# Kernel tuning notes

Measured on AMD Instinct MI355X. Metric: run time of the kernel, lower is better.

Reference implementation:

```python
import jax, jax.numpy as jnp
import numpy as np

L, B, H, R = 128, 4, 768, 24
LN_EPS = 1e-5


def setup_inputs() -> dict:
    key = jax.random.key(0)
    ks = jax.random.split(key, 10)
    s = 1.0 / np.sqrt(H)
    return {
        "h_re": jax.random.normal(ks[0], (L, B, H), jnp.float32),
        "h_share": jax.random.normal(ks[1], (L, B, H), jnp.float32),
        "mask": jnp.ones((L, B), jnp.float32),
        # r: Linear(2H -> H)
        "r_w": jax.random.normal(ks[2], (H, 2 * H), jnp.float32) * s,
        "r_b": jnp.zeros((H,), jnp.float32),
        # hid2hid: Linear(3H -> H)
        "hid_w": jax.random.normal(ks[3], (H, 3 * H), jnp.float32) * s,
        "hid_b": jnp.zeros((H,), jnp.float32),
        # LayerNorm(H)
        "ln_g": jnp.ones((H,), jnp.float32),
        "ln_b": jnp.zeros((H,), jnp.float32),
        # hid2rel: Linear(H -> R)
        "rel_w": jax.random.normal(ks[4], (R, H), jnp.float32) * s,
        "rel_b": jnp.zeros((R,), jnp.float32),
    }


def reference(h_re, h_share, mask, r_w, r_b, hid_w, hid_b, ln_g, ln_b, rel_w, rel_b):
    # h_global = max_over_length( tanh( Linear([h_share; h_re]) ) )  -> [B, H]
    # Decompose concat-linear into two additive projections (same math).
    w_sh, w_re = r_w[:, :H], r_w[:, H:]
    g = jnp.tanh(jnp.einsum('lbh,kh->lbk', h_share, w_sh)
                 + jnp.einsum('lbh,kh->lbk', h_re, w_re) + r_b)
    g = jnp.max(g, axis=0)  # [B, H]

    # hid2hid(cat(r1, r2, g)) = h_re@W1^T (bcast over j) + h_re@W2^T (bcast over i) + g@W3^T + b
    w1, w2, w3 = hid_w[:, :H], hid_w[:, H:2 * H], hid_w[:, 2 * H:]
    p1 = jnp.einsum('lbh,kh->lbk', h_re, w1)        # [L, B, H] -> varies with i
    p2 = jnp.einsum('lbh,kh->lbk', h_re, w2)        # [L, B, H] -> varies with j
    pg = jnp.einsum('bh,kh->bk', g, w3) + hid_b     # [B, H]
    z = p1[:, None, :, :] + p2[None, :, :, :] + pg  # [L, L, B, H]

    # LayerNorm over last dim
    mu = jnp.mean(z, axis=-1, keepdims=True)
    var = jnp.mean(jnp.square(z - mu), axis=-1, keepdims=True)
    z = (z - mu) * jax.lax.rsqrt(var + LN_EPS) * ln_g + ln_b

    # ELU (dropout = identity in eval), then sigmoid(hid2rel)
    z = jax.nn.elu(z)
    re = jax.nn.sigmoid(jnp.einsum('ijbh,rh->ijbr', z, rel_w) + rel_b)  # [L, L, B, R]

    # pairwise mask: mask[i,b] * mask[j,b]
    m = mask[:, None, :] * mask[None, :, :]        # [L, L, B]
    return re * m[..., None]
```

## Files before the change

kernel.cpp:

```cpp
#include <hip/hip_runtime.h>
#include <hip/hip_bf16.h>
#include <math.h>

#define L 128
#define B 4
#define H 768
#define LN_EPS 1e-5f
#define XROWS 272
#define DSTRIDE 73984

typedef __attribute__((ext_vector_type(8))) short short8;
typedef __attribute__((ext_vector_type(4))) float f32x4;
typedef __attribute__((ext_vector_type(16))) float f32x16;

static __device__ __forceinline__ unsigned f2bfu(float f) {
    unsigned u = __float_as_uint(f);
    return (u + 0x7FFFu + ((u >> 16) & 1u)) >> 16;
}
static __device__ __forceinline__ uint2 pk4(float4 v) {
    uint2 o;
    o.x = f2bfu(v.x) | (f2bfu(v.y) << 16);
    o.y = f2bfu(v.z) | (f2bfu(v.w) << 16);
    return o;
}
static __device__ __forceinline__ unsigned short f2b(float f) {
    union { __hip_bfloat16 h; unsigned short u; } cv;
    cv.h = __float2bfloat16(f);
    return cv.u;
}
static __device__ __forceinline__ float4 unpk4(uint2 p) {
    return make_float4(__uint_as_float(p.x << 16),
                       __uint_as_float(p.x & 0xffff0000u),
                       __uint_as_float(p.y << 16),
                       __uint_as_float(p.y & 0xffff0000u));
}
static __device__ __forceinline__ unsigned fkey(float x) {
    unsigned u = __float_as_uint(x);
    return (u >> 31) ? ~u : (u | 0x80000000u);
}

__global__ __launch_bounds__(256) void kConv(const float* __restrict__ h_re,
                                             const float* __restrict__ h_share,
                                             const float* __restrict__ r_w,
                                             const float* __restrict__ hid_w,
                                             const float* __restrict__ rel_w,
                                             unsigned short* __restrict__ apack,
                                             unsigned short* __restrict__ wpackA,
                                             unsigned short* __restrict__ wpackB,
                                             unsigned short* __restrict__ rwb2,
                                             unsigned short* __restrict__ xb16,
                                             unsigned int* __restrict__ gmax) {
    int t = blockIdx.x * 256 + threadIdx.x;
    if (t >= 402816) return;
    if (t < 98304) {
        int m = t / 192, oct = t % 192, k = oct * 8;
        const float* src = (k < 768) ? (h_share + (size_t)m * 768 + k)
                                     : (h_re + (size_t)m * 768 + k - 768);
        float4 x = *(const float4*)src, y = *(const float4*)(src + 4);
        int mt = m >> 4, lr = m & 15, ks = k >> 5, lq = (k >> 3) & 3;
        uint2* dst = (uint2*)(apack + (((size_t)mt * 48 + ks) * 64 + lq * 16 + lr) * 8);
        dst[0] = pk4(x); dst[1] = pk4(y);
    } else if (t < 245760) {
        int t2 = t - 98304;
        int n = t2 / 192, oct = t2 % 192, k = oct * 8;
        const float* src = r_w + (size_t)n * 1536 + k;
        float4 x = *(const float4*)src, y = *(const float4*)(src + 4);
        int nt = n >> 4, lr = n & 15, ks = k >> 5, lq = (k >> 3) & 3;
        uint2* dst = (uint2*)(wpackA + (((size_t)nt * 48 + ks) * 64 + lq * 16 + lr) * 8);
        dst[0] = pk4(x); dst[1] = pk4(y);
    } else if (t < 393216) {
        int t3 = t - 245760;
        int n = t3 / 96, oct = t3 % 96, k = oct * 8;
        int half = (n >= 768) ? 1 : 0;
        const float* src = hid_w + (size_t)(n - half * 768) * 2304 + half * 768 + k;
        float4 x = *(const float4*)src, y = *(const float4*)(src + 4);
        int nt = n >> 4, lr = n & 15, ks = k >> 5, lq = (k >> 3) & 3;
        uint2* dst = (uint2*)(wpackB + (((size_t)nt * 24 + ks) * 64 + lq * 16 + lr) * 8);
        dst[0] = pk4(x); dst[1] = pk4(y);
    } else if (t < 396288) {
        int t4 = t - 393216;
        int s = t4 >> 6, l = t4 & 63;
        int row = l & 31;
        uint2 o0 = make_uint2(0u, 0u), o1 = o0;
        if (row < 24) {
            const float* src = rel_w + (size_t)row * 768 + s * 16 + (l >> 5) * 8;
            o0 = pk4(*(const float4*)src);
            o1 = pk4(*(const float4*)(src + 4));
        }
        uint2* dst = (uint2*)(rwb2 + (size_t)t4 * 8);
        dst[0] = o0; dst[1] = o1;
    } else if (t < 402048) {
        int t5 = t - 396288;
        int b = t5 / 1440, rem = t5 % 1440, row = 257 + rem / 96, oct = rem % 96;
        unsigned val = (row == 257) ? 0x3F803F80u : 0u;
        uint2* dst = (uint2*)(xb16 + ((size_t)b * XROWS + row) * 768 + oct * 8);
        dst[0] = make_uint2(val, val); dst[1] = make_uint2(val, val);
    } else {
        int t6 = t - 402048;
        ((uint4*)gmax)[t6] = make_uint4(0u, 0u, 0u, 0u);
    }
}

template<int KS>
static __device__ __forceinline__ void gemm_tile(const unsigned short* __restrict__ ap,
                                                 const unsigned short* __restrict__ wr,
                                                 f32x4 acc[2][2]) {
#pragma unroll 8
    for (int s = 0; s < KS; s++) {
        short8 a0 = *(const short8*)(ap + (size_t)s * 512);
        short8 a1 = *(const short8*)(ap + (size_t)(48 + s) * 512);
        short8 w0 = *(const short8*)(wr + (size_t)s * 512);
        short8 w1 = *(const short8*)(wr + (size_t)(KS + s) * 512);
        acc[0][0] = __builtin_amdgcn_mfma_f32_16x16x32_bf16(a0, w0, acc[0][0], 0, 0, 0);
        acc[0][1] = __builtin_amdgcn_mfma_f32_16x16x32_bf16(a0, w1, acc[0][1], 0, 0, 0);
        acc[1][0] = __builtin_amdgcn_mfma_f32_16x16x32_bf16(a1, w0, acc[1][0], 0, 0, 0);
        acc[1][1] = __builtin_amdgcn_mfma_f32_16x16x32_bf16(a1, w1, acc[1][1], 0, 0, 0);
    }
}

__global__ __launch_bounds__(64) void kGemm(const unsigned short* __restrict__ apack,
                                            const unsigned short* __restrict__ wpackA,
                                            const unsigned short* __restrict__ wpackB,
                                            unsigned int* __restrict__ gmax,
                                            unsigned short* __restrict__ xb16) {
    int id = blockIdx.x;
    int lane = threadIdx.x;
    int lq = lane >> 4, lr = lane & 15;
    f32x4 acc[2][2] = {{{0.f,0.f,0.f,0.f},{0.f,0.f,0.f,0.f}},
                       {{0.f,0.f,0.f,0.f},{0.f,0.f,0.f,0.f}}};
    if (id < 384) {
        int mt0 = (id / 24) * 2, nt0 = (id % 24) * 2;
        const unsigned short* ap = apack + (size_t)mt0 * 48 * 512 + lane * 8;
        const unsigned short* wr = wpackA + (size_t)nt0 * 48 * 512 + lane * 8;
        gemm_tile<48>(ap, wr, acc);
#pragma unroll
        for (int ni = 0; ni < 2; ni++)
#pragma unroll
            for (int q = 0; q < 4; q++) {
                float mx = fmaxf(acc[0][ni][q], acc[1][ni][q]);
                mx = fmaxf(mx, __shfl_xor(mx, 16, 64));
                mx = fmaxf(mx, __shfl_xor(mx, 32, 64));
                if (lq == 0) {
                    int n = (nt0 + ni) * 16 + lr;
                    atomicMax(&gmax[q * 768 + n], fkey(mx));
                }
            }
    } else {
        int id2 = id - 384;
        int mt0 = (id2 / 48) * 2, nt0 = (id2 % 48) * 2;
        const unsigned short* ap = apack + ((size_t)mt0 * 48 + 24) * 512 + lane * 8;
        const unsigned short* wr = wpackB + (size_t)nt0 * 24 * 512 + lane * 8;
        gemm_tile<24>(ap, wr, acc);
#pragma unroll
        for (int mi = 0; mi < 2; mi++)
#pragma unroll
            for (int ni = 0; ni < 2; ni++)
#pragma unroll
                for (int q = 0; q < 4; q++) {
                    int m = (mt0 + mi) * 16 + lq * 4 + q;
                    int n = (nt0 + ni) * 16 + lr;
                    int b = m & 3, l = m >> 2;
                    size_t row = (n < 768) ? (size_t)l : (size_t)(128 + l);
                    int col = (n < 768) ? n : n - 768;
                    xb16[((size_t)b * XROWS + row) * 768 + col] = f2b(acc[mi][ni][q]);
                }
    }
}

__global__ __launch_bounds__(256) void kPg(const unsigned int* __restrict__ gmax,
                                           const float* __restrict__ r_b,
                                           const float* __restrict__ hid_w,
                                           const float* __restrict__ hid_b,
                                           unsigned short* __restrict__ xb16) {
    __shared__ float sg[768];
    __shared__ float sp[4][64];
    int kt = blockIdx.x, b = blockIdx.y, tid = threadIdx.x;
    for (int v = tid; v < 768; v += 256) {
        unsigned key = gmax[b * 768 + v];
        unsigned bits = (key & 0x80000000u) ? (key & 0x7FFFFFFFu) : ~key;
        sg[v] = tanhf(__uint_as_float(bits) + r_b[v]);
    }
    __syncthreads();
    int kk = tid & 63, hc = tid >> 6;
    int k = kt * 64 + kk;
    const float4* w4 = (const float4*)hid_w;
    const float4* g4 = (const float4*)sg;
    float acc = 0.f;
    for (int h = hc * 48; h < hc * 48 + 48; h++) {
        float4 gv = g4[h];
        float4 wv = w4[(size_t)k * 576 + 384 + h];
        acc += gv.x * wv.x + gv.y * wv.y + gv.z * wv.z + gv.w * wv.w;
    }
    sp[hc][kk] = acc;
    __syncthreads();
    if (hc == 0) {
        float pgv = sp[0][kk] + sp[1][kk] + sp[2][kk] + sp[3][kk] + hid_b[k];
        xb16[((size_t)b * XROWS + 256) * 768 + k] = f2b(pgv);
    }
}

__global__ __launch_bounds__(256) void kPack(const unsigned short* __restrict__ xb16,
                                             unsigned short* __restrict__ xpack) {
    int t = blockIdx.x * 256 + threadIdx.x;
    int b = t / 26112, rem = t % 26112;
    int r = rem / 96, k8 = rem % 96;
    const uint2* src = (const uint2*)(xb16 + ((size_t)b * XROWS + r) * 768 + k8 * 8);
    uint2 v0 = src[0], v1 = src[1];
    size_t dst = ((((size_t)(b * 17 + (r >> 4)) * 24 + (k8 >> 2)) * 64)
                  + (k8 & 3) * 16 + (r & 15)) * 8;
    uint2* d = (uint2*)(xpack + dst);
    d[0] = v0; d[1] = v1;
}

__global__ __launch_bounds__(64) void kGram(const unsigned short* __restrict__ xpack,
                                            float* __restrict__ D) {
    int it = blockIdx.x, jt = blockIdx.y, b = blockIdx.z;
    int lane = threadIdx.x, lq = lane >> 4, lr = lane & 15;
    const unsigned short* ar = xpack + ((size_t)(b * 17 + it) * 24 * 64 + lane) * 8;
    const unsigned short* wr = xpack + ((size_t)(b * 17 + jt) * 24 * 64 + lane) * 8;
    f32x4 acc = {0.f, 0.f, 0.f, 0.f};
#pragma unroll 8
    for (int s = 0; s < 24; s++) {
        short8 a = *(const short8*)(ar + (size_t)s * 512);
        short8 w = *(const short8*)(wr + (size_t)s * 512);
        acc = __builtin_amdgcn_mfma_f32_16x16x32_bf16(a, w, acc, 0, 0, 0);
    }
    float* Db = D + (size_t)b * DSTRIDE;
#pragma unroll
    for (int q = 0; q < 4; q++)
        Db[(size_t)(it * 16 + lq * 4 + q) * XROWS + jt * 16 + lr] = acc[q];
}

__global__ __launch_bounds__(512, 6) void kC(const unsigned short* __restrict__ xb16,
                                             const float* __restrict__ ln_g,
                                             const float* __restrict__ ln_b,
                                             const unsigned short* __restrict__ rwb2,
                                             const float* __restrict__ rel_b,
                                             const float* __restrict__ D,
                                             const float* __restrict__ mask,
                                             float* __restrict__ out) {
    __shared__ __align__(16) unsigned char smem[49920];
    __shared__ float smu[32], srs[32];
    unsigned short (*zls)[780] = (unsigned short (*)[780])smem;
    int i = blockIdx.x, b = blockIdx.y, j0 = blockIdx.z * 32;
    int tid = threadIdx.x, lane = tid & 63, wave = tid >> 6;

    if (tid < 32) {
        const float* Db = D + (size_t)b * DSTRIDE;
        int vr = 128 + j0 + tid;
        float Su1 = Db[(size_t)i * XROWS + 257];
        float Su2 = Db[(size_t)i * XROWS + i];
        float up  = Db[(size_t)i * XROWS + 256];
        float Sp1 = Db[(size_t)256 * XROWS + 257];
        float Sp2 = Db[(size_t)256 * XROWS + 256];
        float Sv1 = Db[(size_t)vr * XROWS + 257];
        float Sv2 = Db[(size_t)vr * XROWS + vr];
        float Dij = Db[(size_t)i * XROWS + vr];
        float cvj = Db[(size_t)vr * XROWS + 256];
        float s1 = Su1 + Sp1 + Sv1;
        float s2 = Su2 + Sp2 + Sv2 + 2.f * (Dij + up + cvj);
        float mu = s1 * (1.f / 768.f);
        smu[tid] = mu;
        srs[tid] = rsqrtf(s2 * (1.f / 768.f) - mu * mu + LN_EPS);
    }
    const uint2* ur = (const uint2*)(xb16 + ((size_t)b * XROWS + i) * 768);
    const uint2* pr = (const uint2*)(xb16 + ((size_t)b * XROWS + 256) * 768);
    const float4* lg4 = (const float4*)ln_g;
    const float4* lb4 = (const float4*)ln_b;
    float4 t1[3], gg[3], bb[3];
#pragma unroll
    for (int s = 0; s < 3; s++) {
        int c = lane + 64 * s;
        float4 x = unpk4(ur[c]), y = unpk4(pr[c]);
        t1[s] = make_float4(x.x + y.x, x.y + y.y, x.z + y.z, x.w + y.w);
        gg[s] = lg4[c];
        bb[s] = lb4[c];
    }
    __syncthreads();

#pragma unroll
    for (int jj = 0; jj < 4; jj++) {
        int j = wave * 4 + jj;
        float mu = smu[j], rs = srs[j];
        const uint2* vr2 = (const uint2*)(xb16 + ((size_t)b * XROWS + 128 + j0 + j) * 768);
        uint2* zrow = (uint2*)&zls[j][0];
#pragma unroll
        for (int s = 0; s < 3; s++) {
            int c = lane + 64 * s;
            float4 vv = unpk4(vr2[c]);
            float A0 = rs * gg[s].x, A1 = rs * gg[s].y, A2 = rs * gg[s].z, A3 = rs * gg[s].w;
            float C0 = fmaf(-mu, A0, bb[s].x), C1 = fmaf(-mu, A1, bb[s].y);
            float C2 = fmaf(-mu, A2, bb[s].z), C3 = fmaf(-mu, A3, bb[s].w);
            float z0 = fmaf(t1[s].x + vv.x, A0, C0);
            float z1 = fmaf(t1[s].y + vv.y, A1, C1);
            float z2 = fmaf(t1[s].z + vv.z, A2, C2);
            float z3 = fmaf(t1[s].w + vv.w, A3, C3);
            z0 = fmaxf(z0, __expf(fminf(z0, 0.f)) - 1.f);
            z1 = fmaxf(z1, __expf(fminf(z1, 0.f)) - 1.f);
            z2 = fmaxf(z2, __expf(fminf(z2, 0.f)) - 1.f);
            z3 = fmaxf(z3, __expf(fminf(z3, 0.f)) - 1.f);
            uint2 o;
            o.x = (unsigned)f2b(z0) | ((unsigned)f2b(z1) << 16);
            o.y = (unsigned)f2b(z2) | ((unsigned)f2b(z3) << 16);
            zrow[c] = o;
        }
    }
    __syncthreads();

    int arow = lane & 31, ahi = lane >> 5;
    f32x16 acc = {0.f,0.f,0.f,0.f, 0.f,0.f,0.f,0.f, 0.f,0.f,0.f,0.f, 0.f,0.f,0.f,0.f};
    const unsigned short* bptr = rwb2 + ((size_t)(wave * 6) * 64 + lane) * 8;
#pragma unroll
    for (int st = 0; st < 6; st++) {
        int s = wave * 6 + st;
        short8 a  = *(const short8*)&zls[arow][s * 16 + ahi * 8];
        short8 bf = *(const short8*)(bptr + (size_t)st * 512);
        acc = __builtin_amdgcn_mfma_f32_32x32x16_bf16(a, bf, acc, 0, 0, 0);
    }
    __syncthreads();
    float* pf = (float*)smem;
#pragma unroll
    for (int r = 0; r < 16; r++) {
        int row = (r & 3) + 8 * (r >> 2) + 4 * ahi;
        pf[wave * 1024 + row * 32 + arow] = acc[r];
    }
    __syncthreads();

#pragma unroll
    for (int e0 = 0; e0 < 2; e0++) {
        int e = tid + e0 * 512;
        int row = e >> 5, col = e & 31;
        if (col < 24) {
            float v = 0.f;
#pragma unroll
            for (int w = 0; w < 8; w++) v += pf[w * 1024 + e];
            int jgl = j0 + row;
            float mval = mask[i * 4 + b] * mask[jgl * 4 + b];
            out[((size_t)(i * 128 + jgl) * 4 + b) * 24 + col] =
                mval / (1.f + __expf(-(v + rel_b[col])));
        }
    }
}

extern "C" void kernel_launch(void* const* d_in, const int* in_sizes, int n_in,
                              void* d_out, int out_size, void* d_ws, size_t ws_size,
                              hipStream_t stream) {
    const float* h_re    = (const float*)d_in[0];
    const float* h_share = (const float*)d_in[1];
    const float* mask    = (const float*)d_in[2];
    const float* r_w     = (const float*)d_in[3];
    const float* r_b     = (const float*)d_in[4];
    const float* hid_w   = (const float*)d_in[5];
    const float* hid_b   = (const float*)d_in[6];
    const float* ln_g    = (const float*)d_in[7];
    const float* ln_b    = (const float*)d_in[8];
    const float* rel_w   = (const float*)d_in[9];
    const float* rel_b   = (const float*)d_in[10];
    float* out = (float*)d_out;

    float* ws = (float*)d_ws;
    unsigned short* apack  = (unsigned short*)(ws);
    unsigned short* wpackA = (unsigned short*)(ws + 393216);
    unsigned short* wpackB = (unsigned short*)(ws + 983040);
    unsigned short* xb16   = (unsigned short*)(ws + 1572864);
    float*          D      = ws + 1990656;
    unsigned int*   gmax   = (unsigned int*)(ws + 2286592);
    unsigned short* rwb2   = (unsigned short*)(ws + 2289664);
    unsigned short* xpack  = (unsigned short*)(ws);

    kConv<<<1574, 256, 0, stream>>>(h_re, h_share, r_w, hid_w, rel_w,
                                    apack, wpackA, wpackB, rwb2, xb16, gmax);
    kGemm<<<1152, 64, 0, stream>>>(apack, wpackA, wpackB, gmax, xb16);
    kPg<<<dim3(12, 4), 256, 0, stream>>>(gmax, r_b, hid_w, hid_b, xb16);
    kPack<<<408, 256, 0, stream>>>(xb16, xpack);
    kGram<<<dim3(17, 17, 4), 64, 0, stream>>>(xpack, D);
    kC<<<dim3(L, B, 4), 512, 0, stream>>>(xb16, ln_g, ln_b, rwb2, rel_b,
                                          D, mask, out);
}
```

Before: 77.12 us.

## Fuse pg projection with xpack packing and compute only needed Gram tiles

Merges the pg-vector kernel and the pack kernel into one launch. The pg row, the ones row and the zero rows of the last 16-row tile are now written straight into the packed layout, so kConv no longer initialises the padding rows of xb16. kGram now launches only the 97 tile pairs that kC appears to read (the cross block between i and j halves, the diagonal tiles, and the tiles against the pg/ones tile) instead of all 17x17 per batch. This removes one launch and redundant MFMA tiles. It relies on kC never reading the Gram entries or xb16 padding rows that are no longer written.

```diff
diff --git a/kernel.cpp b/kernel.cpp
--- a/kernel.cpp
+++ b/kernel.cpp
@@ -48,10 +48,9 @@
                                              unsigned short* __restrict__ wpackA,
                                              unsigned short* __restrict__ wpackB,
                                              unsigned short* __restrict__ rwb2,
-                                             unsigned short* __restrict__ xb16,
                                              unsigned int* __restrict__ gmax) {
     int t = blockIdx.x * 256 + threadIdx.x;
-    if (t >= 402816) return;
+    if (t >= 397056) return;
     if (t < 98304) {
         int m = t / 192, oct = t % 192, k = oct * 8;
         const float* src = (k < 768) ? (h_share + (size_t)m * 768 + k)
@@ -89,15 +88,12 @@
         }
         uint2* dst = (uint2*)(rwb2 + (size_t)t4 * 8);
         dst[0] = o0; dst[1] = o1;
-    } else if (t < 402048) {
-        int t5 = t - 396288;
-        int b = t5 / 1440, rem = t5 % 1440, row = 257 + rem / 96, oct = rem % 96;
-        unsigned val = (row == 257) ? 0x3F803F80u : 0u;
-        uint2* dst = (uint2*)(xb16 + ((size_t)b * XROWS + row) * 768 + oct * 8);
-        dst[0] = make_uint2(val, val); dst[1] = make_uint2(val, val);
     } else {
-        int t6 = t - 402048;
-        ((uint4*)gmax)[t6] = make_uint4(0u, 0u, 0u, 0u);
+        int t6 = t - 396288;
+        gmax[t6] = 0u;
+        gmax[768 + t6] = 0u;
+        gmax[1536 + t6] = 0u;
+        gmax[2304 + t6] = 0u;
     }
 }
 
@@ -167,14 +163,29 @@
     }
 }
 
-__global__ __launch_bounds__(256) void kPg(const unsigned int* __restrict__ gmax,
-                                           const float* __restrict__ r_b,
-                                           const float* __restrict__ hid_w,
-                                           const float* __restrict__ hid_b,
-                                           unsigned short* __restrict__ xb16) {
+__global__ __launch_bounds__(256) void kPgPack(const unsigned int* __restrict__ gmax,
+                                               const float* __restrict__ r_b,
+                                               const float* __restrict__ hid_w,
+                                               const float* __restrict__ hid_b,
+                                               unsigned short* xb16,
+                                               unsigned short* __restrict__ xpack) {
+    int blk = blockIdx.x, tid = threadIdx.x;
+    if (blk >= 48) {
+        int t = (blk - 48) * 256 + tid;
+        int b = t / 24576, rem = t % 24576;
+        int r = rem / 96, k8 = rem % 96;
+        const uint2* src = (const uint2*)(xb16 + ((size_t)b * XROWS + r) * 768 + k8 * 8);
+        uint2 v0 = src[0], v1 = src[1];
+        size_t dst = ((((size_t)(b * 17 + (r >> 4)) * 24 + (k8 >> 2)) * 64)
+                      + (k8 & 3) * 16 + (r & 15)) * 8;
+        uint2* d = (uint2*)(xpack + dst);
+        d[0] = v0; d[1] = v1;
+        return;
+    }
     __shared__ float sg[768];
     __shared__ float sp[4][64];
-    int kt = blockIdx.x, b = blockIdx.y, tid = threadIdx.x;
+    __shared__ float spg[64];
+    int kt = blk % 12, b = blk / 12;
     for (int v = tid; v < 768; v += 256) {
         unsigned key = gmax[b * 768 + v];
         unsigned bits = (key & 0x80000000u) ? (key & 0x7FFFFFFFu) : ~key;
@@ -195,26 +206,39 @@
     __syncthreads();
     if (hc == 0) {
         float pgv = sp[0][kk] + sp[1][kk] + sp[2][kk] + sp[3][kk] + hid_b[k];
+        spg[kk] = pgv;
         xb16[((size_t)b * XROWS + 256) * 768 + k] = f2b(pgv);
     }
-}
-
-__global__ __launch_bounds__(256) void kPack(const unsigned short* __restrict__ xb16,
-                                             unsigned short* __restrict__ xpack) {
-    int t = blockIdx.x * 256 + threadIdx.x;
-    int b = t / 26112, rem = t % 26112;
-    int r = rem / 96, k8 = rem % 96;
-    const uint2* src = (const uint2*)(xb16 + ((size_t)b * XROWS + r) * 768 + k8 * 8);
-    uint2 v0 = src[0], v1 = src[1];
-    size_t dst = ((((size_t)(b * 17 + (r >> 4)) * 24 + (k8 >> 2)) * 64)
-                  + (k8 & 3) * 16 + (r & 15)) * 8;
-    uint2* d = (uint2*)(xpack + dst);
-    d[0] = v0; d[1] = v1;
+    __syncthreads();
+    if (tid < 128) {
+        int ksl = tid >> 6, lane = tid & 63;
+        int ks = kt * 2 + ksl;
+        int row16 = lane & 15;
+        int kbase = ksl * 32 + (lane >> 4) * 8;
+        unsigned short vals[8];
+        if (row16 == 0) {
+#pragma unroll
+            for (int e = 0; e < 8; e++) vals[e] = f2b(spg[kbase + e]);
+        } else if (row16 == 1) {
+#pragma unroll
+            for (int e = 0; e < 8; e++) vals[e] = 0x3F80;
+        } else {
+#pragma unroll
+            for (int e = 0; e < 8; e++) vals[e] = 0;
+        }
+        uint2* d = (uint2*)(xpack + (((size_t)(b * 17 + 16) * 24 + ks) * 64 + lane) * 8);
+        d[0] = *(uint2*)&vals[0];
+        d[1] = *(uint2*)&vals[4];
+    }
 }
 
 __global__ __launch_bounds__(64) void kGram(const unsigned short* __restrict__ xpack,
                                             float* __restrict__ D) {
-    int it = blockIdx.x, jt = blockIdx.y, b = blockIdx.z;
+    int t = blockIdx.x, b = blockIdx.y;
+    int it, jt;
+    if (t < 64)      { it = t >> 3;  jt = 8 + (t & 7); }
+    else if (t < 80) { it = t - 64;  jt = t - 64; }
+    else             { it = t - 80;  jt = 16; }
     int lane = threadIdx.x, lq = lane >> 4, lr = lane & 15;
     const unsigned short* ar = xpack + ((size_t)(b * 17 + it) * 24 * 64 + lane) * 8;
     const unsigned short* wr = xpack + ((size_t)(b * 17 + jt) * 24 * 64 + lane) * 8;
@@ -368,12 +392,11 @@
     unsigned short* rwb2   = (unsigned short*)(ws + 2289664);
     unsigned short* xpack  = (unsigned short*)(ws);
 
-    kConv<<<1574, 256, 0, stream>>>(h_re, h_share, r_w, hid_w, rel_w,
-                                    apack, wpackA, wpackB, rwb2, xb16, gmax);
+    kConv<<<1552, 256, 0, stream>>>(h_re, h_share, r_w, hid_w, rel_w,
+                                    apack, wpackA, wpackB, rwb2, gmax);
     kGemm<<<1152, 64, 0, stream>>>(apack, wpackA, wpackB, gmax, xb16);
-    kPg<<<dim3(12, 4), 256, 0, stream>>>(gmax, r_b, hid_w, hid_b, xb16);
-    kPack<<<408, 256, 0, stream>>>(xb16, xpack);
-    kGram<<<dim3(17, 17, 4), 64, 0, stream>>>(xpack, D);
+    kPgPack<<<432, 256, 0, stream>>>(gmax, r_b, hid_w, hid_b, xb16, xpack);
+    kGram<<<dim3(97, 4), 64, 0, stream>>>(xpack, D);
     kC<<<dim3(L, B, 4), 512, 0, stream>>>(xb16, ln_g, ln_b, rwb2, rel_b,
                                           D, mask, out);
 }
```

After: 73.46 us. -4.7%, faster.
